# Kernel tuning notes

Hardware: AMD Instinct MI355X
Metric: run time of the kernel (lower is better)

## Reference

```python
import jax, jax.numpy as jnp
import numpy as np

# Dims: B batch, CK key dim, CV value dim, NOBJ objects, T memory frames, HxW feature map
B, CK, CV, NOBJ, T, H, W = 1, 64, 512, 2, 2, 64, 64


def setup_inputs() -> dict:
    key = jax.random.key(0)
    k1, k2, k3, k4, k5 = jax.random.split(key, 5)
    return {
        "query_key": jax.random.normal(k1, (B, CK, H, W), jnp.float32),
        "query_selection": jax.random.uniform(k2, (B, CK, H, W), jnp.float32),
        "memory_key": jax.random.normal(k3, (B, CK, T, H, W), jnp.float32),
        "memory_shrinkage": jax.random.uniform(k4, (B, 1, T, H, W), jnp.float32),
        "memory_value": jax.random.normal(k5, (B, NOBJ, CV, T, H, W), jnp.float32),
    }


def reference(query_key, query_selection, memory_key, memory_shrinkage, memory_value):
    b, nobj, cv = memory_value.shape[:3]
    ck = memory_key.shape[1]
    h, w = query_key.shape[-2:]
    hw = h * w
    mk = memory_key.reshape(b, ck, -1)            # (b, ck, N) with N = T*H*W
    ms = memory_shrinkage.reshape(b, -1)          # (b, N)
    qk = query_key.reshape(b, ck, hw)             # (b, ck, hw)
    qe = query_selection.reshape(b, ck, hw)       # (b, ck, hw)
    mv = memory_value.reshape(b, nobj * cv, -1)   # (b, nobj*cv, N)

    # Negative L2 similarity with selection weighting (XMem get_similarity)
    a_sq = jnp.einsum('bcn,bcp->bnp', mk * mk, qe)            # (b, N, hw)
    two_ab = 2.0 * jnp.einsum('bcn,bcp->bnp', mk, qk * qe)    # (b, N, hw)
    b_sq = jnp.sum(qe * qk * qk, axis=1, keepdims=True)       # (b, 1, hw)
    inv_sqrt_ck = np.float32(1.0 / np.sqrt(ck))
    sim = (two_ab - a_sq - b_sq) * ms[:, :, None] * inv_sqrt_ck

    # Softmax over memory slots (dim N), then weighted readout
    aff = jax.nn.softmax(sim, axis=1)                          # (b, N, hw)
    mem = jnp.einsum('bvn,bnp->bvp', mv, aff)                  # (b, nobj*cv, hw)
    return mem.reshape(b, nobj, cv, h, w)
```

## Files before the change

### kernel.cpp

```cpp
#include <hip/hip_runtime.h>
#include <stdint.h>

typedef unsigned short u16;
typedef __attribute__((ext_vector_type(4))) float f32x4;
typedef __attribute__((ext_vector_type(8))) __bf16 bf16x8;
typedef __attribute__((ext_vector_type(4))) unsigned int u32x4;

#define HWPX 4096
#define NMEM 8192
#define CKD  64
#define VROWS 1024

__device__ __forceinline__ u16 f2bf(float x) {
    union { float f; unsigned u; } v; v.f = x;
    unsigned r = v.u + 0x7FFFu + ((v.u >> 16) & 1u);
    return (u16)(r >> 16);
}
__device__ __forceinline__ float bf2f(u16 h) {
    union { unsigned u; float f; } v; v.u = ((unsigned)h) << 16;
    return v.f;
}

__device__ __forceinline__ void gld_lds16(const void* g, void* l) {
    __builtin_amdgcn_global_load_lds(
        (const __attribute__((address_space(1))) uint32_t*)g,
        (__attribute__((address_space(3))) uint32_t*)l, 16, 0, 0);
}

__global__ void prep_q(const float* __restrict__ qk, const float* __restrict__ qe,
                       u16* __restrict__ Qhat, float* __restrict__ bsq) {
    int p = blockIdx.x * 256 + threadIdx.x;
    float acc = 0.f;
    #pragma unroll 4
    for (int c = 0; c < CKD; ++c) {
        float k = qk[c * HWPX + p];
        float e = qe[c * HWPX + p];
        Qhat[p * 128 + c]      = f2bf(k * e);
        Qhat[p * 128 + 64 + c] = f2bf(e);
        acc += e * k * k;
    }
    bsq[p] = acc;
}

__global__ void prep_k(const float* __restrict__ mk, u16* __restrict__ Khat) {
    int n = blockIdx.x * 256 + threadIdx.x;
    #pragma unroll 4
    for (int c = 0; c < CKD; ++c) {
        float m = mk[c * NMEM + n];
        Khat[n * 128 + c]      = f2bf(2.f * m);
        Khat[n * 128 + 64 + c] = f2bf(-m * m);
    }
}

__global__ void prep_mv(const float* __restrict__ mv, u16* __restrict__ mvb) {
    int i = blockIdx.x * 256 + threadIdx.x;
    float4 v = ((const float4*)mv)[i];
    u16 o0 = f2bf(v.x), o1 = f2bf(v.y), o2 = f2bf(v.z), o3 = f2bf(v.w);
    unsigned lo = (unsigned)o0 | ((unsigned)o1 << 16);
    unsigned hi = (unsigned)o2 | ((unsigned)o3 << 16);
    ((uint2*)mvb)[i] = make_uint2(lo, hi);
}

__launch_bounds__(256)
__global__ void gemm1_kernel(const u16* __restrict__ Qhat, const u16* __restrict__ Khat,
                             const float* __restrict__ bsq, const float* __restrict__ ms,
                             u16* __restrict__ Pt, float* __restrict__ denom) {
    __shared__ __align__(16) u16 smem[32768];
    u16* Qs = smem;
    u16* Ks = smem + 16384;

    const int tid  = threadIdx.x;
    const int l    = tid & 63;
    const int w    = tid >> 6;
    const int quad = l >> 4;
    const int l15  = l & 15;
    const int wm = w >> 1, wn = w & 1;
    const int p0 = blockIdx.x * 128;
    const int n0 = blockIdx.y * 128;

    {
        const int rsub = tid >> 4;
        const int csw  = (tid & 15) ^ (rsub & 15);
        #pragma unroll
        for (int rnd = 0; rnd < 8; ++rnd) {
            gld_lds16(Qhat + (size_t)(p0 + rnd * 16 + rsub) * 128 + csw * 8,
                      Qs + rnd * 2048 + w * 512);
            gld_lds16(Khat + (size_t)(n0 + rnd * 16 + rsub) * 128 + csw * 8,
                      Ks + rnd * 2048 + w * 512);
        }
    }
    __syncthreads();

    f32x4 acc[4][4] = {};
    #pragma unroll
    for (int kk = 0; kk < 4; ++kk) {
        bf16x8 a[4], b[4];
        #pragma unroll
        for (int mi = 0; mi < 4; ++mi) {
            int row = wm * 64 + mi * 16 + l15;
            a[mi] = *(const bf16x8*)(Qs + row * 128 + (((kk * 4 + quad) ^ l15) << 3));
        }
        #pragma unroll
        for (int ni = 0; ni < 4; ++ni) {
            int row = wn * 64 + ni * 16 + l15;
            b[ni] = *(const bf16x8*)(Ks + row * 128 + (((kk * 4 + quad) ^ l15) << 3));
        }
        #pragma unroll
        for (int mi = 0; mi < 4; ++mi)
            #pragma unroll
            for (int ni = 0; ni < 4; ++ni)
                acc[mi][ni] = __builtin_amdgcn_mfma_f32_16x16x32_bf16(a[mi], b[ni], acc[mi][ni], 0, 0, 0);
    }

    float msv[4];
    #pragma unroll
    for (int ni = 0; ni < 4; ++ni)
        msv[ni] = ms[n0 + wn * 64 + ni * 16 + l15] * 0.125f;
    float bsv[4][4];
    #pragma unroll
    for (int mi = 0; mi < 4; ++mi)
        #pragma unroll
        for (int r = 0; r < 4; ++r)
            bsv[mi][r] = bsq[p0 + wm * 64 + mi * 16 + quad * 4 + r];

    __syncthreads();
    u16* Ps = smem;
    #pragma unroll
    for (int mi = 0; mi < 4; ++mi) {
        #pragma unroll
        for (int ni = 0; ni < 4; ++ni) {
            f32x4 v = acc[mi][ni];
            int col = wn * 64 + ni * 16 + l15;
            #pragma unroll
            for (int r = 0; r < 4; ++r) {
                int rowl = wm * 64 + mi * 16 + quad * 4 + r;
                float sim = (v[r] - bsv[mi][r]) * msv[ni];
                Ps[rowl * 136 + col] = f2bf(__expf(sim));
            }
        }
    }
    __syncthreads();

    if (tid < 128) {
        float s = 0.f;
        #pragma unroll 8
        for (int jj = 0; jj < 128; ++jj) {
            int j = (jj + 2 * tid) & 127;
            s += bf2f(Ps[tid * 136 + j]);
        }
        atomicAdd(&denom[p0 + tid], s);
    }

    {
        int row = tid >> 1, half = tid & 1;
        const u32x4* src = (const u32x4*)(Ps + row * 136 + half * 64);
        u32x4* dst = (u32x4*)(Pt + (size_t)(p0 + row) * NMEM + n0 + half * 64);
        #pragma unroll
        for (int i = 0; i < 8; ++i) dst[i] = src[i];
    }
}

__launch_bounds__(256, 4)
__global__ void gemm2_kernel(const u16* __restrict__ Ab, const u16* __restrict__ Bt,
                             float* __restrict__ outacc) {
    __shared__ __align__(16) u16 As[128 * 64];
    __shared__ __align__(16) u16 Bs[128 * 64];

    const int tid  = threadIdx.x;
    const int l    = tid & 63;
    const int w    = tid >> 6;
    const int quad = l >> 4;
    const int l15  = l & 15;
    const int wm = w >> 1, wn = w & 1;
    const int v0 = blockIdx.x * 128;
    const int p0 = blockIdx.y * 128;
    const int kbeg = blockIdx.z * (NMEM / 4);
    const int kend = kbeg + (NMEM / 4);
    const int rsub = tid >> 3;
    const int csw  = (tid & 7) ^ (rsub & 7);

    f32x4 acc[4][4] = {};

    for (int k0 = kbeg; k0 < kend; k0 += 64) {
        __syncthreads();
        #pragma unroll
        for (int rnd = 0; rnd < 4; ++rnd) {
            gld_lds16(Ab + (size_t)(v0 + rnd * 32 + rsub) * NMEM + k0 + csw * 8,
                      As + rnd * 2048 + w * 512);
            gld_lds16(Bt + (size_t)(p0 + rnd * 32 + rsub) * NMEM + k0 + csw * 8,
                      Bs + rnd * 2048 + w * 512);
        }
        __syncthreads();
        #pragma unroll
        for (int kk = 0; kk < 2; ++kk) {
            bf16x8 a[4], b[4];
            #pragma unroll
            for (int mi = 0; mi < 4; ++mi) {
                int row = wm * 64 + mi * 16 + l15;
                a[mi] = *(const bf16x8*)(As + row * 64 + (((kk * 4 + quad) ^ (l15 & 7)) << 3));
            }
            #pragma unroll
            for (int ni = 0; ni < 4; ++ni) {
                int row = wn * 64 + ni * 16 + l15;
                b[ni] = *(const bf16x8*)(Bs + row * 64 + (((kk * 4 + quad) ^ (l15 & 7)) << 3));
            }
            #pragma unroll
            for (int mi = 0; mi < 4; ++mi)
                #pragma unroll
                for (int ni = 0; ni < 4; ++ni)
                    acc[mi][ni] = __builtin_amdgcn_mfma_f32_16x16x32_bf16(a[mi], b[ni], acc[mi][ni], 0, 0, 0);
        }
    }

    #pragma unroll
    for (int mi = 0; mi < 4; ++mi) {
        #pragma unroll
        for (int ni = 0; ni < 4; ++ni) {
            int col = p0 + wn * 64 + ni * 16 + l15;
            f32x4 v = acc[mi][ni];
            #pragma unroll
            for (int r = 0; r < 4; ++r) {
                int row = v0 + wm * 64 + mi * 16 + quad * 4 + r;
                atomicAdd(&outacc[(size_t)row * HWPX + col], v[r]);
            }
        }
    }
}

__global__ void divide_out(float* __restrict__ out, const float* __restrict__ denom) {
    int f = blockIdx.x * 256 + threadIdx.x;
    float4 v = ((float4*)out)[f];
    int p4 = f & (HWPX / 4 - 1);
    float4 d = ((const float4*)denom)[p4];
    v.x /= d.x; v.y /= d.y; v.z /= d.z; v.w /= d.w;
    ((float4*)out)[f] = v;
}

extern "C" void kernel_launch(void* const* d_in, const int* in_sizes, int n_in,
                              void* d_out, int out_size, void* d_ws, size_t ws_size,
                              hipStream_t stream) {
    const float* qk = (const float*)d_in[0];
    const float* qe = (const float*)d_in[1];
    const float* mk = (const float*)d_in[2];
    const float* ms = (const float*)d_in[3];
    const float* mv = (const float*)d_in[4];
    float* out = (float*)d_out;

    char* ws = (char*)d_ws;
    u16*   Pt    = (u16*)ws;
    u16*   mvb   = (u16*)(ws + ((size_t)64 << 20));
    u16*   Khat  = (u16*)(ws + ((size_t)80 << 20));
    u16*   Qhat  = (u16*)(ws + ((size_t)82 << 20));
    float* bsq   = (float*)(ws + ((size_t)83 << 20));
    float* denom = (float*)(ws + ((size_t)83 << 20) + 65536);

    hipMemsetAsync(denom, 0, HWPX * sizeof(float), stream);
    hipMemsetAsync(out, 0, (size_t)VROWS * HWPX * sizeof(float), stream);
    prep_q<<<HWPX / 256, 256, 0, stream>>>(qk, qe, Qhat, bsq);
    prep_k<<<NMEM / 256, 256, 0, stream>>>(mk, Khat);
    prep_mv<<<(VROWS * NMEM / 4) / 256, 256, 0, stream>>>(mv, mvb);

    dim3 g1(HWPX / 128, NMEM / 128);
    gemm1_kernel<<<g1, 256, 0, stream>>>(Qhat, Khat, bsq, ms, Pt, denom);

    dim3 g2(VROWS / 128, HWPX / 128, 4);
    gemm2_kernel<<<g2, 256, 0, stream>>>(mvb, Pt, out);

    divide_out<<<(VROWS * HWPX / 4) / 256, 256, 0, stream>>>(out, denom);
}
```

Measured before the change: 267.7 us.

## Tile P layout, register row sums, swizzled gemm2 grid with deeper split-K

gemm1 now sums the softmax numerators in registers with wave shuffles and skips the LDS rescan, so the denominator uses fp32 exp values instead of the bf16-rounded ones. It also writes the P matrix as contiguous 128x128 tiles rather than row-major across all memory slots. gemm2 reads those tiles, remaps block indices so blocks sharing the same P tiles are grouped, and doubles split-K from 4 to 8. Its launch bound also rises to 5 blocks per SM. The goal is better locality and more parallelism in the second GEMM, at the cost of twice as many fp32 atomic output accumulations.

```diff
diff --git a/kernel.cpp b/kernel.cpp
--- a/kernel.cpp
+++ b/kernel.cpp
@@ -15,10 +15,6 @@
     union { float f; unsigned u; } v; v.f = x;
     unsigned r = v.u + 0x7FFFu + ((v.u >> 16) & 1u);
     return (u16)(r >> 16);
-}
-__device__ __forceinline__ float bf2f(u16 h) {
-    union { unsigned u; float f; } v; v.u = ((unsigned)h) << 16;
-    return v.f;
 }
 
 __device__ __forceinline__ void gld_lds16(const void* g, void* l) {
@@ -125,6 +121,7 @@
 
     __syncthreads();
     u16* Ps = smem;
+    float rowsum[4][4] = {};
     #pragma unroll
     for (int mi = 0; mi < 4; ++mi) {
         #pragma unroll
@@ -134,33 +131,43 @@
             #pragma unroll
             for (int r = 0; r < 4; ++r) {
                 int rowl = wm * 64 + mi * 16 + quad * 4 + r;
-                float sim = (v[r] - bsv[mi][r]) * msv[ni];
-                Ps[rowl * 136 + col] = f2bf(__expf(sim));
-            }
-        }
+                float pv = __expf((v[r] - bsv[mi][r]) * msv[ni]);
+                rowsum[mi][r] += pv;
+                Ps[rowl * 136 + col] = f2bf(pv);
+            }
+        }
+    }
+    #pragma unroll
+    for (int mi = 0; mi < 4; ++mi)
+        #pragma unroll
+        for (int r = 0; r < 4; ++r) {
+            float s = rowsum[mi][r];
+            s += __shfl_xor(s, 1);
+            s += __shfl_xor(s, 2);
+            s += __shfl_xor(s, 4);
+            s += __shfl_xor(s, 8);
+            rowsum[mi][r] = s;
+        }
+    if (l15 == 0) {
+        #pragma unroll
+        for (int mi = 0; mi < 4; ++mi)
+            #pragma unroll
+            for (int r = 0; r < 4; ++r)
+                atomicAdd(&denom[p0 + wm * 64 + mi * 16 + quad * 4 + r], rowsum[mi][r]);
     }
     __syncthreads();
 
-    if (tid < 128) {
-        float s = 0.f;
-        #pragma unroll 8
-        for (int jj = 0; jj < 128; ++jj) {
-            int j = (jj + 2 * tid) & 127;
-            s += bf2f(Ps[tid * 136 + j]);
-        }
-        atomicAdd(&denom[p0 + tid], s);
-    }
-
     {
+        const size_t tileOff = ((size_t)blockIdx.x * 64 + blockIdx.y) * 16384;
         int row = tid >> 1, half = tid & 1;
         const u32x4* src = (const u32x4*)(Ps + row * 136 + half * 64);
-        u32x4* dst = (u32x4*)(Pt + (size_t)(p0 + row) * NMEM + n0 + half * 64);
+        u32x4* dst = (u32x4*)(Pt + tileOff + row * 128 + half * 64);
         #pragma unroll
         for (int i = 0; i < 8; ++i) dst[i] = src[i];
     }
 }
 
-__launch_bounds__(256, 4)
+__launch_bounds__(256, 5)
 __global__ void gemm2_kernel(const u16* __restrict__ Ab, const u16* __restrict__ Bt,
                              float* __restrict__ outacc) {
     __shared__ __align__(16) u16 As[128 * 64];
@@ -172,22 +179,31 @@
     const int quad = l >> 4;
     const int l15  = l & 15;
     const int wm = w >> 1, wn = w & 1;
-    const int v0 = blockIdx.x * 128;
-    const int p0 = blockIdx.y * 128;
-    const int kbeg = blockIdx.z * (NMEM / 4);
-    const int kend = kbeg + (NMEM / 4);
+
+    const int lin = blockIdx.x + (blockIdx.y << 3) + (blockIdx.z << 8);
+    const int vb  = (lin >> 3) & 7;
+    const int pb  = (lin & 7) | (((lin >> 6) & 3) << 3);
+    const int kz  = lin >> 8;
+    const int v0 = vb * 128;
+    const int p0 = pb * 128;
+    const int kbeg = kz * (NMEM / 8);
+    const int kend = kbeg + (NMEM / 8);
+
     const int rsub = tid >> 3;
     const int csw  = (tid & 7) ^ (rsub & 7);
 
     f32x4 acc[4][4] = {};
 
     for (int k0 = kbeg; k0 < kend; k0 += 64) {
+        const int nb = k0 >> 7;
+        const int nh = (k0 >> 6) & 1;
+        const u16* bsrc = Bt + ((size_t)pb * 64 + nb) * 16384 + nh * 64;
         __syncthreads();
         #pragma unroll
         for (int rnd = 0; rnd < 4; ++rnd) {
             gld_lds16(Ab + (size_t)(v0 + rnd * 32 + rsub) * NMEM + k0 + csw * 8,
                       As + rnd * 2048 + w * 512);
-            gld_lds16(Bt + (size_t)(p0 + rnd * 32 + rsub) * NMEM + k0 + csw * 8,
+            gld_lds16(bsrc + (rnd * 32 + rsub) * 128 + csw * 8,
                       Bs + rnd * 2048 + w * 512);
         }
         __syncthreads();
@@ -263,7 +279,7 @@
     dim3 g1(HWPX / 128, NMEM / 128);
     gemm1_kernel<<<g1, 256, 0, stream>>>(Qhat, Khat, bsq, ms, Pt, denom);
 
-    dim3 g2(VROWS / 128, HWPX / 128, 4);
+    dim3 g2(8, 32, 8);
     gemm2_kernel<<<g2, 256, 0, stream>>>(mvb, Pt, out);
 
     divide_out<<<(VROWS * HWPX / 4) / 256, 256, 0, stream>>>(out, denom);
```

Result: slower. 302.7 us (+13.1%).
